# Kernel optimization log

Measured on AMD Instinct MI355X. Metric: run time of the kernel, lower is better.

Reference implementation:

```python
import jax, jax.numpy as jnp
import numpy as np

N, M, D = 32768, 4096, 512  # batch, m*n prototypes, prototype dim


def setup_inputs() -> dict:
    key = jax.random.key(0)
    k1, k2 = jax.random.split(key)
    z = jax.random.normal(k1, (N, D), dtype=jnp.float32)
    prototypes = jax.random.normal(k2, (M, D), dtype=jnp.float32)
    return {"z": z, "prototypes": prototypes}


def reference(z, prototypes):
    # Squared euclidean distances via GEMM expansion:
    #   ||z - p||^2 = ||z||^2 - 2 z.p + ||p||^2
    z2 = jnp.sum(z * z, axis=1, keepdims=True)            # [N,1]
    p2 = jnp.sum(prototypes * prototypes, axis=1)         # [M]
    d2 = z2 - 2.0 * (z @ prototypes.T) + p2[None, :]      # [N,M]
    min_idx = jnp.argmin(d2, axis=1)                      # same argmin as cdist
    winner_prototypes = prototypes[min_idx]               # [N,D]
    return winner_prototypes, min_idx
```

## Files before the change

### kernel.cpp

```cpp
#include <hip/hip_runtime.h>


#define N_ROWS 32768
#define M_PROTO 4096
#define DIM 512

typedef _Float16 half8 __attribute__((ext_vector_type(8)));
typedef _Float16 half4_t __attribute__((ext_vector_type(4)));
typedef float f32x4 __attribute__((ext_vector_type(4)));

__device__ __forceinline__ void gl_lds16(const void* g, void* l) {
    __builtin_amdgcn_global_load_lds(
        (const __attribute__((address_space(1))) unsigned int*)g,
        (__attribute__((address_space(3))) unsigned int*)l, 16, 0, 0);
}

__global__ __launch_bounds__(256) void p2_kernel(const float* __restrict__ p,
                                                 float* __restrict__ p2) {
    const int w = threadIdx.x >> 6, l = threadIdx.x & 63;
    const int m = blockIdx.x * 4 + w;
    const float4* p4 = (const float4*)p + (size_t)m * 128;
    float s = 0.f;
#pragma unroll
    for (int i = 0; i < 2; ++i) {
        float4 v = p4[l * 2 + i];
        s += v.x * v.x + v.y * v.y + v.z * v.z + v.w * v.w;
    }
#pragma unroll
    for (int mm = 1; mm < 64; mm <<= 1) s += __shfl_xor(s, mm);
    if (l == 0) p2[m] = s;
}

__global__ __launch_bounds__(256) void conv_p_kernel(const float* __restrict__ p,
                                                     _Float16* __restrict__ ph,
                                                     _Float16* __restrict__ pl) {
    const int tile = blockIdx.x;
    const int bi = tile >> 3, kt = tile & 7;
    const float4* p4 = (const float4*)p;
    const size_t tb = (size_t)tile * 8192;
#pragma unroll
    for (int it = 0; it < 8; ++it) {
        int q = it * 256 + threadIdx.x;
        int row = q >> 4, kq = q & 15;
        float4 v = p4[(size_t)(bi * 128 + row) * 128 + kt * 16 + kq];
        _Float16 h0 = (_Float16)v.x, h1 = (_Float16)v.y;
        _Float16 h2 = (_Float16)v.z, h3 = (_Float16)v.w;
        half4_t hv = {h0, h1, h2, h3};
        half4_t lv = {(_Float16)(v.x - (float)h0), (_Float16)(v.y - (float)h1),
                      (_Float16)(v.z - (float)h2), (_Float16)(v.w - (float)h3)};
        int addr = row * 64 + (((kq >> 1) ^ (row & 7)) << 3) + ((kq & 1) << 2);
        *(half4_t*)&ph[tb + addr] = hv;
        *(half4_t*)&pl[tb + addr] = lv;
    }
}

__global__ __launch_bounds__(256, 1) void som_main(
    const float* __restrict__ z,
    const _Float16* __restrict__ ph, const _Float16* __restrict__ pl,
    const float* __restrict__ p2, const float* __restrict__ prot,
    float* __restrict__ out) {
    __shared__ __align__(16) _Float16 sPH[2][8192];
    __shared__ __align__(16) _Float16 sPL[2][8192];
    __shared__ int sFI[128];

    const int tid = threadIdx.x;
    const int w = tid >> 6, l = tid & 63;
    const int g = l >> 4, c = l & 15;
    const int blk = blockIdx.x, brow = blk * 128;

    half8 za[2][16], zb[2][16];
#pragma unroll
    for (int st = 0; st < 2; ++st) {
        const int rowg = brow + (w * 2 + st) * 16 + c;
        const float4* zr = (const float4*)z + (size_t)rowg * 128;
#pragma unroll
        for (int ks = 0; ks < 16; ++ks) {
            float4 v0 = zr[ks * 8 + g * 2 + 0];
            float4 v1 = zr[ks * 8 + g * 2 + 1];
            float x0 = -2.f * v0.x, x1 = -2.f * v0.y, x2 = -2.f * v0.z, x3 = -2.f * v0.w;
            float x4 = -2.f * v1.x, x5 = -2.f * v1.y, x6 = -2.f * v1.z, x7 = -2.f * v1.w;
            _Float16 h0 = (_Float16)x0, h1 = (_Float16)x1, h2 = (_Float16)x2, h3 = (_Float16)x3;
            _Float16 h4 = (_Float16)x4, h5 = (_Float16)x5, h6 = (_Float16)x6, h7 = (_Float16)x7;
            half8 hv = {h0, h1, h2, h3, h4, h5, h6, h7};
            half8 lv = {(_Float16)(x0 - (float)h0), (_Float16)(x1 - (float)h1),
                        (_Float16)(x2 - (float)h2), (_Float16)(x3 - (float)h3),
                        (_Float16)(x4 - (float)h4), (_Float16)(x5 - (float)h5),
                        (_Float16)(x6 - (float)h6), (_Float16)(x7 - (float)h7)};
            za[st][ks] = hv;
            zb[st][ks] = lv;
        }
    }

#pragma unroll
    for (int j = 0; j < 4; ++j) {
        const int off = j * 2048 + tid * 8;
        gl_lds16(ph + off, &sPH[0][off]);
        gl_lds16(pl + off, &sPL[0][off]);
    }
    __syncthreads();

    float minv[2][4];
    int mini[2][4];
#pragma unroll
    for (int st = 0; st < 2; ++st)
#pragma unroll
        for (int r = 0; r < 4; ++r) { minv[st][r] = 3.0e38f; mini[st][r] = 0; }

    for (int bi = 0; bi < 32; ++bi) {
        f32x4 acc[2][8];
#pragma unroll
        for (int st = 0; st < 2; ++st)
#pragma unroll
            for (int jt = 0; jt < 8; ++jt) acc[st][jt] = (f32x4){0.f, 0.f, 0.f, 0.f};

#pragma unroll
        for (int kt = 0; kt < 8; ++kt) {
            const int cur = kt & 1;
            const int tp = bi * 8 + kt;
            if (tp < 255) {
                const _Float16* sph = ph + (size_t)(tp + 1) * 8192;
                const _Float16* spl = pl + (size_t)(tp + 1) * 8192;
#pragma unroll
                for (int j = 0; j < 4; ++j) {
                    const int off = j * 2048 + tid * 8;
                    gl_lds16(sph + off, &sPH[cur ^ 1][off]);
                    gl_lds16(spl + off, &sPL[cur ^ 1][off]);
                }
            }
#pragma unroll
            for (int ksl = 0; ksl < 2; ++ksl) {
                const int ks = kt * 2 + ksl;
#pragma unroll
                for (int jt = 0; jt < 8; ++jt) {
                    const int row = jt * 16 + c;
                    const int addr = row * 64 + (((ksl * 4 + g) ^ (row & 7)) << 3);
                    half8 bh = *(half8*)&sPH[cur][addr];
                    half8 bl = *(half8*)&sPL[cur][addr];
#pragma unroll
                    for (int st = 0; st < 2; ++st) {
                        acc[st][jt] = __builtin_amdgcn_mfma_f32_16x16x32_f16(za[st][ks], bh, acc[st][jt], 0, 0, 0);
                        acc[st][jt] = __builtin_amdgcn_mfma_f32_16x16x32_f16(za[st][ks], bl, acc[st][jt], 0, 0, 0);
                        acc[st][jt] = __builtin_amdgcn_mfma_f32_16x16x32_f16(zb[st][ks], bh, acc[st][jt], 0, 0, 0);
                    }
                }
            }
            __syncthreads();
        }

#pragma unroll
        for (int jt = 0; jt < 8; ++jt) {
            const int colg = bi * 128 + jt * 16 + c;
            float pv = p2[colg];
#pragma unroll
            for (int st = 0; st < 2; ++st)
#pragma unroll
                for (int r = 0; r < 4; ++r) {
                    float s = acc[st][jt][r] + pv;
                    if (s < minv[st][r] || (s == minv[st][r] && colg < mini[st][r])) {
                        minv[st][r] = s;
                        mini[st][r] = colg;
                    }
                }
        }
    }

#pragma unroll
    for (int st = 0; st < 2; ++st)
#pragma unroll
        for (int r = 0; r < 4; ++r) {
            float v = minv[st][r];
            int id = mini[st][r];
#pragma unroll
            for (int mm = 1; mm < 16; mm <<= 1) {
                float ov = __shfl_xor(v, mm);
                int oi = __shfl_xor(id, mm);
                if (ov < v || (ov == v && oi < id)) { v = ov; id = oi; }
            }
            if (c == 0) {
                const int rl = (w * 2 + st) * 16 + g * 4 + r;
                sFI[rl] = id;
                out[(size_t)N_ROWS * DIM + brow + rl] = (float)id;
            }
        }
    __syncthreads();

    const float4* pr4 = (const float4*)prot;
    float4* out4 = (float4*)out;
#pragma unroll 4
    for (int it = 0; it < 64; ++it) {
        const int q = it * 256 + tid;
        const int row = q >> 7, qk = q & 127;
        const int fi = sFI[row];
        out4[(size_t)(brow + row) * 128 + qk] = pr4[(size_t)fi * 128 + qk];
    }
}

__global__ __launch_bounds__(256) void som_fallback(const float* __restrict__ z,
                                                    const float* __restrict__ prot,
                                                    const float* __restrict__ p2,
                                                    float* __restrict__ out) {
    __shared__ __align__(16) _Float16 sZH[64 * 64];
    __shared__ __align__(16) _Float16 sZL[64 * 64];
    __shared__ __align__(16) _Float16 sPH[128 * 64];
    __shared__ __align__(16) _Float16 sPL[128 * 64];
    __shared__ float sMV[4][64];
    __shared__ int sMI[4][64];
    __shared__ int sFI[64];

    const int tid = threadIdx.x;
    const int w = tid >> 6, l = tid & 63;
    const int g = l >> 4, c = l & 15;
    const int brow = blockIdx.x * 64;
    const float4* z4 = (const float4*)z;
    const float4* pr4 = (const float4*)prot;

    float minv[4][4];
    int mini[4][4];
#pragma unroll
    for (int i = 0; i < 4; ++i)
#pragma unroll
        for (int r = 0; r < 4; ++r) { minv[i][r] = 3.0e38f; mini[i][r] = 0; }

    for (int bcol = 0; bcol < M_PROTO; bcol += 128) {
        f32x4 acc[4][2];
#pragma unroll
        for (int i = 0; i < 4; ++i)
#pragma unroll
            for (int jt = 0; jt < 2; ++jt) acc[i][jt] = (f32x4){0.f, 0.f, 0.f, 0.f};
        for (int kt = 0; kt < 8; ++kt) {
            __syncthreads();
#pragma unroll
            for (int it = 0; it < 4; ++it) {
                int q = it * 256 + tid;
                int row = q >> 4, kq = q & 15;
                float4 v = z4[(size_t)(brow + row) * 128 + kt * 16 + kq];
                float x0 = -2.f * v.x, x1 = -2.f * v.y, x2 = -2.f * v.z, x3 = -2.f * v.w;
                _Float16 h0 = (_Float16)x0, h1 = (_Float16)x1;
                _Float16 h2 = (_Float16)x2, h3 = (_Float16)x3;
                half4_t hv = {h0, h1, h2, h3};
                half4_t lv = {(_Float16)(x0 - (float)h0), (_Float16)(x1 - (float)h1),
                              (_Float16)(x2 - (float)h2), (_Float16)(x3 - (float)h3)};
                int addr = row * 64 + (((kq >> 1) ^ (row & 7)) << 3) + ((kq & 1) << 2);
                *(half4_t*)&sZH[addr] = hv;
                *(half4_t*)&sZL[addr] = lv;
            }
#pragma unroll
            for (int it = 0; it < 8; ++it) {
                int q = it * 256 + tid;
                int row = q >> 4, kq = q & 15;
                float4 v = pr4[(size_t)(bcol + row) * 128 + kt * 16 + kq];
                _Float16 h0 = (_Float16)v.x, h1 = (_Float16)v.y;
                _Float16 h2 = (_Float16)v.z, h3 = (_Float16)v.w;
                half4_t hv = {h0, h1, h2, h3};
                half4_t lv = {(_Float16)(v.x - (float)h0), (_Float16)(v.y - (float)h1),
                              (_Float16)(v.z - (float)h2), (_Float16)(v.w - (float)h3)};
                int addr = row * 64 + (((kq >> 1) ^ (row & 7)) << 3) + ((kq & 1) << 2);
                *(half4_t*)&sPH[addr] = hv;
                *(half4_t*)&sPL[addr] = lv;
            }
            __syncthreads();
#pragma unroll
            for (int ks = 0; ks < 2; ++ks) {
                half8 ah[4], al[4], bh[2], bl[2];
#pragma unroll
                for (int i = 0; i < 4; ++i) {
                    int row = i * 16 + c;
                    int addr = row * 64 + (((ks * 4 + g) ^ (row & 7)) << 3);
                    ah[i] = *(half8*)&sZH[addr];
                    al[i] = *(half8*)&sZL[addr];
                }
#pragma unroll
                for (int jt = 0; jt < 2; ++jt) {
                    int row = w * 32 + jt * 16 + c;
                    int addr = row * 64 + (((ks * 4 + g) ^ (row & 7)) << 3);
                    bh[jt] = *(half8*)&sPH[addr];
                    bl[jt] = *(half8*)&sPL[addr];
                }
#pragma unroll
                for (int i = 0; i < 4; ++i)
#pragma unroll
                    for (int jt = 0; jt < 2; ++jt) {
                        acc[i][jt] = __builtin_amdgcn_mfma_f32_16x16x32_f16(ah[i], bh[jt], acc[i][jt], 0, 0, 0);
                        acc[i][jt] = __builtin_amdgcn_mfma_f32_16x16x32_f16(ah[i], bl[jt], acc[i][jt], 0, 0, 0);
                        acc[i][jt] = __builtin_amdgcn_mfma_f32_16x16x32_f16(al[i], bh[jt], acc[i][jt], 0, 0, 0);
                    }
            }
        }
#pragma unroll
        for (int jt = 0; jt < 2; ++jt) {
            int colg = bcol + w * 32 + jt * 16 + c;
            float pv = p2[colg];
#pragma unroll
            for (int i = 0; i < 4; ++i)
#pragma unroll
                for (int r = 0; r < 4; ++r) {
                    float s = acc[i][jt][r] + pv;
                    if (s < minv[i][r] || (s == minv[i][r] && colg < mini[i][r])) {
                        minv[i][r] = s;
                        mini[i][r] = colg;
                    }
                }
        }
    }
#pragma unroll
    for (int i = 0; i < 4; ++i)
#pragma unroll
        for (int r = 0; r < 4; ++r) {
            float v = minv[i][r];
            int id = mini[i][r];
#pragma unroll
            for (int mm = 1; mm < 16; mm <<= 1) {
                float ov = __shfl_xor(v, mm);
                int oi = __shfl_xor(id, mm);
                if (ov < v || (ov == v && oi < id)) { v = ov; id = oi; }
            }
            if (c == 0) {
                sMV[w][i * 16 + g * 4 + r] = v;
                sMI[w][i * 16 + g * 4 + r] = id;
            }
        }
    __syncthreads();
    if (tid < 64) {
        float v = sMV[0][tid];
        int id = sMI[0][tid];
#pragma unroll
        for (int ww = 1; ww < 4; ++ww) {
            float ov = sMV[ww][tid];
            int oi = sMI[ww][tid];
            if (ov < v || (ov == v && oi < id)) { v = ov; id = oi; }
        }
        sFI[tid] = id;
        out[(size_t)N_ROWS * DIM + brow + tid] = (float)id;
    }
    __syncthreads();
    float4* out4 = (float4*)out;
#pragma unroll 4
    for (int it = 0; it < 32; ++it) {
        int q = it * 256 + tid;
        int row = q >> 7, qk = q & 127;
        int fi = sFI[row];
        out4[(size_t)(brow + row) * 128 + qk] = pr4[(size_t)fi * 128 + qk];
    }
}

extern "C" void kernel_launch(void* const* d_in, const int* in_sizes, int n_in,
                              void* d_out, int out_size, void* d_ws, size_t ws_size,
                              hipStream_t stream) {
    const float* z = (const float*)d_in[0];
    const float* prot = (const float*)d_in[1];
    char* base = (char*)d_ws;
    float* p2 = (float*)base;

    const size_t NEED = 16384 + 8388608;

    p2_kernel<<<M_PROTO / 4, 256, 0, stream>>>(prot, p2);

    if (ws_size >= NEED) {
        _Float16* ph = (_Float16*)(base + 16384);
        _Float16* pl = (_Float16*)(base + 16384 + 4194304);
        conv_p_kernel<<<256, 256, 0, stream>>>(prot, ph, pl);
        som_main<<<N_ROWS / 128, 256, 0, stream>>>(z, ph, pl, p2, prot, (float*)d_out);
    } else {
        som_fallback<<<N_ROWS / 64, 256, 0, stream>>>(z, prot, p2, (float*)d_out);
    }
}
```

Measured before the change: 574.8 us.

## Deepen prototype LDS pipeline to four buffers with prefetch distance two

```diff
diff --git a/kernel.cpp b/kernel.cpp
--- a/kernel.cpp
+++ b/kernel.cpp
@@ -14,6 +14,8 @@
         (const __attribute__((address_space(1))) unsigned int*)g,
         (__attribute__((address_space(3))) unsigned int*)l, 16, 0, 0);
 }
+
+#define WAITV(N) asm volatile("s_waitcnt vmcnt(" #N ")" ::: "memory")
 
 __global__ __launch_bounds__(256) void p2_kernel(const float* __restrict__ p,
                                                  float* __restrict__ p2) {
@@ -59,8 +61,8 @@
     const _Float16* __restrict__ ph, const _Float16* __restrict__ pl,
     const float* __restrict__ p2, const float* __restrict__ prot,
     float* __restrict__ out) {
-    __shared__ __align__(16) _Float16 sPH[2][8192];
-    __shared__ __align__(16) _Float16 sPL[2][8192];
+    __shared__ __align__(16) _Float16 sPH[4][8192];
+    __shared__ __align__(16) _Float16 sPL[4][8192];
     __shared__ int sFI[128];
 
     const int tid = threadIdx.x;
@@ -92,12 +94,16 @@
     }
 
 #pragma unroll
-    for (int j = 0; j < 4; ++j) {
-        const int off = j * 2048 + tid * 8;
-        gl_lds16(ph + off, &sPH[0][off]);
-        gl_lds16(pl + off, &sPL[0][off]);
-    }
-    __syncthreads();
+    for (int t0 = 0; t0 < 2; ++t0) {
+        const _Float16* sph = ph + (size_t)t0 * 8192;
+        const _Float16* spl = pl + (size_t)t0 * 8192;
+#pragma unroll
+        for (int j = 0; j < 4; ++j) {
+            const int off = j * 2048 + tid * 8;
+            gl_lds16(sph + off, &sPH[t0][off]);
+            gl_lds16(spl + off, &sPL[t0][off]);
+        }
+    }
 
     float minv[2][4];
     int mini[2][4];
@@ -115,18 +121,29 @@
 
 #pragma unroll
         for (int kt = 0; kt < 8; ++kt) {
-            const int cur = kt & 1;
             const int tp = bi * 8 + kt;
-            if (tp < 255) {
-                const _Float16* sph = ph + (size_t)(tp + 1) * 8192;
-                const _Float16* spl = pl + (size_t)(tp + 1) * 8192;
+            const int cb = kt & 3;
+            const int nb = (kt + 2) & 3;
+            if (tp + 2 < 256) {
+                const _Float16* sph = ph + (size_t)(tp + 2) * 8192;
+                const _Float16* spl = pl + (size_t)(tp + 2) * 8192;
 #pragma unroll
                 for (int j = 0; j < 4; ++j) {
                     const int off = j * 2048 + tid * 8;
-                    gl_lds16(sph + off, &sPH[cur ^ 1][off]);
-                    gl_lds16(spl + off, &sPL[cur ^ 1][off]);
-                }
-            }
+                    gl_lds16(sph + off, &sPH[nb][off]);
+                    gl_lds16(spl + off, &sPL[nb][off]);
+                }
+            }
+            if (kt < 6) {
+                WAITV(16);
+            } else if (kt == 6) {
+                if (bi < 31) { WAITV(16); } else { WAITV(8); }
+            } else {
+                if (bi < 31) { WAITV(16); } else { WAITV(0); }
+            }
+            __builtin_amdgcn_s_barrier();
+            __builtin_amdgcn_sched_barrier(0);
+
 #pragma unroll
             for (int ksl = 0; ksl < 2; ++ksl) {
                 const int ks = kt * 2 + ksl;
@@ -134,8 +151,8 @@
                 for (int jt = 0; jt < 8; ++jt) {
                     const int row = jt * 16 + c;
                     const int addr = row * 64 + (((ksl * 4 + g) ^ (row & 7)) << 3);
-                    half8 bh = *(half8*)&sPH[cur][addr];
-                    half8 bl = *(half8*)&sPL[cur][addr];
+                    half8 bh = *(half8*)&sPH[cb][addr];
+                    half8 bl = *(half8*)&sPL[cb][addr];
 #pragma unroll
                     for (int st = 0; st < 2; ++st) {
                         acc[st][jt] = __builtin_amdgcn_mfma_f32_16x16x32_f16(za[st][ks], bh, acc[st][jt], 0, 0, 0);
@@ -144,7 +161,6 @@
                     }
                 }
             }
-            __syncthreads();
         }
 
 #pragma unroll
```

Result: no change. 565.5 us (-1.6%).
